# Kernel tuning notes

Measured on AMD Instinct MI355X. Metric: run time of the kernel, lower is better.

## Reference

```python
import jax, jax.numpy as jnp
import numpy as np


def setup_inputs() -> dict:
    key = jax.random.key(0)
    k1, k2 = jax.random.split(key)
    B, Lq, Ls, D = 16, 2048, 2048, 512
    query = jax.random.normal(k1, (B, Lq, D), dtype=jnp.float32)
    support = jax.random.normal(k2, (B, Ls, D), dtype=jnp.float32)
    return {"query": query, "support": support}


def reference(query, support):
    # attn: [B, Lq, Ls] = softmax(query @ support^T, axis=-1)
    logits = jnp.einsum("bqd,bsd->bqs", query, support)
    attn = jax.nn.softmax(logits, axis=-1)
    # attended support: [B, Lq, D]
    attended = jnp.einsum("bqs,bsd->bqd", attn, support)
    # score: [B, Lq] = sum over D of query * attended
    score = jnp.sum(query * attended, axis=-1)
    return score
```

## Files before the change

### kernel.cpp

```cpp
#include <hip/hip_runtime.h>
#include <hip/hip_bf16.h>

#define B_  16
#define LQ  2048
#define LS  2048
#define DD  512
#define BQ  128
#define BS  128
#define BK  64
#define NSB (LS / BS)
#define NKC (DD / BK)
#define NSPLIT 4

static_assert(NKC == 8, "stage>>3 math assumes NKC==8");

typedef short bf16x8 __attribute__((ext_vector_type(8)));
typedef float f32x4  __attribute__((ext_vector_type(4)));

__device__ __forceinline__ void load_lds16(const void* g, void* l) {
  __builtin_amdgcn_global_load_lds((const __attribute__((address_space(1))) void*)g,
                                   (__attribute__((address_space(3))) void*)l,
                                   16, 0, 0);
}

__device__ __forceinline__ unsigned short f2bf(float f) {
  union { float f; unsigned int u; } v; v.f = f;
  unsigned int r = v.u + 0x7fffu + ((v.u >> 16) & 1u);
  return (unsigned short)(r >> 16);
}

__global__ __launch_bounds__(256) void cvt_kernel(const float* __restrict__ Q,
                                                  const float* __restrict__ S,
                                                  unsigned short* __restrict__ Qw,
                                                  unsigned short* __restrict__ Sw,
                                                  int nblk) {
  int blk = blockIdx.x;
  const float* src; unsigned short* dst;
  if (blk < nblk) { src = Q; dst = Qw; } else { src = S; dst = Sw; blk -= nblk; }
  int i = blk * 256 + threadIdx.x;
  float4 f = ((const float4*)src)[i];
  ushort4 u;
  u.x = f2bf(f.x); u.y = f2bf(f.y); u.z = f2bf(f.z); u.w = f2bf(f.w);
  ((ushort4*)dst)[i] = u;
}

__global__ __launch_bounds__(512, 4) void attn_kernel(const unsigned short* __restrict__ Qw,
                                                      const unsigned short* __restrict__ Sw,
                                                      float* __restrict__ out,
                                                      float* __restrict__ pm,
                                                      float* __restrict__ pse,
                                                      float* __restrict__ psel,
                                                      int nsplit) {
  __shared__ __align__(16) unsigned short sQ[2][BQ * BK];
  __shared__ __align__(16) unsigned short sS[2][BS * BK];

  const int pid = blockIdx.x + (blockIdx.y << 4) + (blockIdx.z << 8);
  const int nch = (nsplit << 8) >> 3;
  const int lid = (pid & 7) * nch + (pid >> 3);
  const int qb  = lid & 15;
  const int b   = (lid >> 4) & 15;
  const int spl = lid >> 8;

  const int tid  = threadIdx.x;
  const int w    = tid >> 6;
  const int lane = tid & 63;
  const int h    = w & 1;
  const int g    = w >> 1;
  const int col  = lane & 15;
  const int quad = lane >> 4;
  const int c7   = col & 7;

  const int q0 = qb * BQ;
  const unsigned short* Qb = Qw + (size_t)b * LQ * DD;
  const unsigned short* Sb = Sw + (size_t)b * LS * DD;

  float mst[2] = { -INFINITY, -INFINITY };
  float se[2]  = { 0.f, 0.f };
  float sel[2] = { 0.f, 0.f };

  f32x4 acc[4][2];
#pragma unroll
  for (int st = 0; st < 4; ++st)
#pragma unroll
    for (int qt = 0; qt < 2; ++qt)
      acc[st][qt] = (f32x4){0.f, 0.f, 0.f, 0.f};

  const int rr    = lane >> 3;
  const int cc    = ((lane & 7) ^ rr) * 8;
  const int srow0 = (w & 3) * 32;

  const int sbs = spl * (NSB / nsplit);
  const int nst = (NSB / nsplit) * NKC;

  auto issue_stage = [&](int sb_i, int kc_i, int buf) {
    if (w < 4) {
#pragma unroll
      for (int i = 0; i < 4; ++i) {
        int r0 = srow0 + i * 8;
        load_lds16(Qb + (size_t)(q0 + r0 + rr) * DD + kc_i * BK + cc, &sQ[buf][r0 * BK]);
      }
    } else {
      const int s0i = sb_i * BS;
#pragma unroll
      for (int i = 0; i < 4; ++i) {
        int r0 = srow0 + i * 8;
        load_lds16(Sb + (size_t)(s0i + r0 + rr) * DD + kc_i * BK + cc, &sS[buf][r0 * BK]);
      }
    }
  };

  issue_stage(sbs, 0, 0);
  int cur = 0;

#pragma unroll 1
  for (int t = 0; t < nst; ++t) {
    asm volatile("s_waitcnt lgkmcnt(0)" ::: "memory");
    __builtin_amdgcn_s_barrier();

    const int tn = t + 1;
    if (tn < nst) {
      issue_stage(sbs + (tn >> 3), tn & 7, cur ^ 1);
      asm volatile("s_waitcnt vmcnt(4)" ::: "memory");
    } else {
      asm volatile("s_waitcnt vmcnt(0)" ::: "memory");
    }
    __builtin_amdgcn_s_barrier();
    __builtin_amdgcn_sched_barrier(0);

    const unsigned short* bq = &sQ[cur][0];
    const unsigned short* bs = &sS[cur][0];
    __builtin_amdgcn_s_setprio(1);
#pragma unroll
    for (int kk = 0; kk < 2; ++kk) {
      const int koff = ((kk * 4 + quad) ^ c7) * 8;
      bf16x8 aq[2], asv[4];
#pragma unroll
      for (int qt = 0; qt < 2; ++qt)
        aq[qt] = *(const bf16x8*)&bq[(g * 32 + qt * 16 + col) * BK + koff];
#pragma unroll
      for (int st = 0; st < 4; ++st)
        asv[st] = *(const bf16x8*)&bs[(h * 64 + st * 16 + col) * BK + koff];
#pragma unroll
      for (int st = 0; st < 4; ++st)
#pragma unroll
        for (int qt = 0; qt < 2; ++qt)
          acc[st][qt] = __builtin_amdgcn_mfma_f32_16x16x32_bf16(asv[st], aq[qt], acc[st][qt], 0, 0, 0);
    }
    __builtin_amdgcn_s_setprio(0);
    cur ^= 1;

    if ((t & (NKC - 1)) == NKC - 1) {
#pragma unroll
      for (int qt = 0; qt < 2; ++qt) {
        float lmax = mst[qt];
#pragma unroll
        for (int st = 0; st < 4; ++st)
#pragma unroll
          for (int r = 0; r < 4; ++r)
            lmax = fmaxf(lmax, acc[st][qt][r]);
        lmax = fmaxf(lmax, __shfl_xor(lmax, 16, 64));
        lmax = fmaxf(lmax, __shfl_xor(lmax, 32, 64));
        float alpha = __expf(mst[qt] - lmax);
        float pe = 0.f, pel = 0.f;
#pragma unroll
        for (int st = 0; st < 4; ++st)
#pragma unroll
          for (int r = 0; r < 4; ++r) {
            float l = acc[st][qt][r];
            float e = __expf(l - lmax);
            pe += e;
            pel = fmaf(e, l, pel);
          }
        pe  += __shfl_xor(pe, 16, 64);  pe  += __shfl_xor(pe, 32, 64);
        pel += __shfl_xor(pel, 16, 64); pel += __shfl_xor(pel, 32, 64);
        se[qt]  = fmaf(se[qt],  alpha, pe);
        sel[qt] = fmaf(sel[qt], alpha, pel);
        mst[qt] = lmax;
      }
#pragma unroll
      for (int st = 0; st < 4; ++st)
#pragma unroll
        for (int qt = 0; qt < 2; ++qt)
          acc[st][qt] = (f32x4){0.f, 0.f, 0.f, 0.f};
    }
  }

  __syncthreads();
  float* red = (float*)&sQ[0][0];
  if (quad == 0) {
#pragma unroll
    for (int qt = 0; qt < 2; ++qt) {
      int idx = ((g * 2 + h) * 2 + qt) * 16 + col;
      red[idx]       = mst[qt];
      red[256 + idx] = se[qt];
      red[512 + idx] = sel[qt];
    }
  }
  __syncthreads();
  if (h == 0 && quad == 0) {
#pragma unroll
    for (int qt = 0; qt < 2; ++qt) {
      int i0 = ((g * 2 + 0) * 2 + qt) * 16 + col;
      int i1 = ((g * 2 + 1) * 2 + qt) * 16 + col;
      float m0 = red[i0], m1 = red[i1];
      float M  = fmaxf(m0, m1);
      float a0 = __expf(m0 - M), a1 = __expf(m1 - M);
      float SE  = red[256 + i0] * a0 + red[256 + i1] * a1;
      float SEL = red[512 + i0] * a0 + red[512 + i1] * a1;
      size_t qi = (size_t)b * LQ + q0 + g * 32 + qt * 16 + col;
      if (nsplit == 1) {
        out[qi] = SEL / SE;
      } else {
        pm[qi * NSPLIT + spl]   = M;
        pse[qi * NSPLIT + spl]  = SE;
        psel[qi * NSPLIT + spl] = SEL;
      }
    }
  }
}

__global__ __launch_bounds__(256) void combine_kernel(const float* __restrict__ pm,
                                                      const float* __restrict__ pse,
                                                      const float* __restrict__ psel,
                                                      float* __restrict__ out) {
  int i = blockIdx.x * blockDim.x + threadIdx.x;
  if (i >= B_ * LQ) return;
  float M = -INFINITY;
#pragma unroll
  for (int s = 0; s < NSPLIT; ++s) M = fmaxf(M, pm[i * NSPLIT + s]);
  float SE = 0.f, SEL = 0.f;
#pragma unroll
  for (int s = 0; s < NSPLIT; ++s) {
    float a = __expf(pm[i * NSPLIT + s] - M);
    SE  = fmaf(pse[i * NSPLIT + s],  a, SE);
    SEL = fmaf(psel[i * NSPLIT + s], a, SEL);
  }
  out[i] = SEL / SE;
}

__global__ __launch_bounds__(256) void fallback_kernel(const float* __restrict__ Q,
                                                       const float* __restrict__ S,
                                                       float* __restrict__ out) {
  __shared__ float qv[DD];
  __shared__ float red[256];
  const int b = blockIdx.y, qi = blockIdx.x, tid = threadIdx.x;
  const float* qrow = Q + ((size_t)b * LQ + qi) * DD;
  for (int d = tid; d < DD; d += 256) qv[d] = qrow[d];
  __syncthreads();
  const float* Sb = S + (size_t)b * LS * DD;
  float m = -INFINITY, se = 0.f, sel = 0.f;
  for (int s = tid; s < LS; s += 256) {
    const float* srow = Sb + (size_t)s * DD;
    float dot = 0.f;
    for (int d = 0; d < DD; ++d) dot = fmaf(qv[d], srow[d], dot);
    float mn = fmaxf(m, dot);
    float a = __expf(m - mn);
    float e = __expf(dot - mn);
    se  = se * a + e;
    sel = sel * a + e * dot;
    m = mn;
  }
  red[tid] = m; __syncthreads();
  for (int o = 128; o > 0; o >>= 1) { if (tid < o) red[tid] = fmaxf(red[tid], red[tid + o]); __syncthreads(); }
  float M = red[0]; __syncthreads();
  float a = __expf(m - M); se *= a; sel *= a;
  red[tid] = se; __syncthreads();
  for (int o = 128; o > 0; o >>= 1) { if (tid < o) red[tid] += red[tid + o]; __syncthreads(); }
  float SE = red[0]; __syncthreads();
  red[tid] = sel; __syncthreads();
  for (int o = 128; o > 0; o >>= 1) { if (tid < o) red[tid] += red[tid + o]; __syncthreads(); }
  float SEL = red[0];
  if (tid == 0) out[(size_t)b * LQ + qi] = SEL / SE;
}

extern "C" void kernel_launch(void* const* d_in, const int* in_sizes, int n_in,
                              void* d_out, int out_size, void* d_ws, size_t ws_size,
                              hipStream_t stream) {
  const float* Q = (const float*)d_in[0];
  const float* S = (const float*)d_in[1];
  float* out = (float*)d_out;
  const size_t nelem = (size_t)B_ * LQ * DD;
  const size_t need_base  = 2 * nelem * sizeof(unsigned short);
  const size_t part_elems = (size_t)B_ * LQ * NSPLIT;
  const size_t need_split = need_base + 3 * part_elems * sizeof(float);

  if (ws_size >= need_base) {
    unsigned short* Qw = (unsigned short*)d_ws;
    unsigned short* Sw = Qw + nelem;
    int nblk = (int)(nelem / 4 / 256);
    cvt_kernel<<<2 * nblk, 256, 0, stream>>>(Q, S, Qw, Sw, nblk);
    if (ws_size >= need_split) {
      float* pm   = (float*)(Sw + nelem);
      float* pse  = pm + part_elems;
      float* psel = pse + part_elems;
      attn_kernel<<<dim3(LQ / BQ, B_, NSPLIT), 512, 0, stream>>>(Qw, Sw, out, pm, pse, psel, NSPLIT);
      combine_kernel<<<(B_ * LQ + 255) / 256, 256, 0, stream>>>(pm, pse, psel, out);
    } else {
      attn_kernel<<<dim3(LQ / BQ, B_, 1), 512, 0, stream>>>(Qw, Sw, out, nullptr, nullptr, nullptr, 1);
    }
  } else {
    fallback_kernel<<<dim3(LQ, B_), 256, 0, stream>>>(Q, S, out);
  }
}
```

Baseline: 234.8 us.

## Double the Q and S tile sizes to 256 with larger per-wave register tiles

Grows the block tile from 128x128 to 256x256, so each wave now holds an 8x4 grid of MFMA accumulators instead of 4x2. Each staged LDS chunk is reused for twice as many MFMAs, which cuts global and LDS traffic per FLOP. Launch bounds drop to 2 waves per SIMD, and the block-id decoding, load issue and reduction layout are reworked to match. In exchange, LDS use doubles to 128KB per block, so only one block fits per CU. Register pressure also rises sharply, which risks spills and less latency hiding.

```diff
diff --git a/kernel.cpp b/kernel.cpp
--- a/kernel.cpp
+++ b/kernel.cpp
@@ -5,8 +5,8 @@
 #define LQ  2048
 #define LS  2048
 #define DD  512
-#define BQ  128
-#define BS  128
+#define BQ  256
+#define BS  256
 #define BK  64
 #define NSB (LS / BS)
 #define NKC (DD / BK)
@@ -44,7 +44,7 @@
   ((ushort4*)dst)[i] = u;
 }
 
-__global__ __launch_bounds__(512, 4) void attn_kernel(const unsigned short* __restrict__ Qw,
+__global__ __launch_bounds__(512, 2) void attn_kernel(const unsigned short* __restrict__ Qw,
                                                       const unsigned short* __restrict__ Sw,
                                                       float* __restrict__ out,
                                                       float* __restrict__ pm,
@@ -54,12 +54,12 @@
   __shared__ __align__(16) unsigned short sQ[2][BQ * BK];
   __shared__ __align__(16) unsigned short sS[2][BS * BK];
 
-  const int pid = blockIdx.x + (blockIdx.y << 4) + (blockIdx.z << 8);
-  const int nch = (nsplit << 8) >> 3;
+  const int pid = blockIdx.x + (blockIdx.y << 3) + (blockIdx.z << 7);
+  const int nch = (nsplit << 7) >> 3;
   const int lid = (pid & 7) * nch + (pid >> 3);
-  const int qb  = lid & 15;
-  const int b   = (lid >> 4) & 15;
-  const int spl = lid >> 8;
+  const int qb  = lid & 7;
+  const int b   = (lid >> 3) & 15;
+  const int spl = lid >> 7;
 
   const int tid  = threadIdx.x;
   const int w    = tid >> 6;
@@ -74,42 +74,42 @@
   const unsigned short* Qb = Qw + (size_t)b * LQ * DD;
   const unsigned short* Sb = Sw + (size_t)b * LS * DD;
 
-  float mst[2] = { -INFINITY, -INFINITY };
-  float se[2]  = { 0.f, 0.f };
-  float sel[2] = { 0.f, 0.f };
-
-  f32x4 acc[4][2];
-#pragma unroll
-  for (int st = 0; st < 4; ++st)
-#pragma unroll
-    for (int qt = 0; qt < 2; ++qt)
+  float mst[4] = { -INFINITY, -INFINITY, -INFINITY, -INFINITY };
+  float se[4]  = { 0.f, 0.f, 0.f, 0.f };
+  float sel[4] = { 0.f, 0.f, 0.f, 0.f };
+
+  f32x4 acc[8][4];
+#pragma unroll
+  for (int st = 0; st < 8; ++st)
+#pragma unroll
+    for (int qt = 0; qt < 4; ++qt)
       acc[st][qt] = (f32x4){0.f, 0.f, 0.f, 0.f};
 
-  const int rr    = lane >> 3;
-  const int cc    = ((lane & 7) ^ rr) * 8;
-  const int srow0 = (w & 3) * 32;
+  const int rr = lane >> 3;
+  const int cc = ((lane & 7) ^ rr) * 8;
 
   const int sbs = spl * (NSB / nsplit);
   const int nst = (NSB / nsplit) * NKC;
 
-  auto issue_stage = [&](int sb_i, int kc_i, int buf) {
+  auto issue_stage = [&](int t_i, int buf) {
+    const int kc = t_i & 7;
     if (w < 4) {
-#pragma unroll
-      for (int i = 0; i < 4; ++i) {
-        int r0 = srow0 + i * 8;
-        load_lds16(Qb + (size_t)(q0 + r0 + rr) * DD + kc_i * BK + cc, &sQ[buf][r0 * BK]);
-      }
+      const unsigned short* gp = Qb + (size_t)(q0 + w * 64 + rr) * DD + kc * BK + cc;
+      unsigned short* lp = &sQ[buf][(w * 64) * BK];
+#pragma unroll
+      for (int i = 0; i < 8; ++i)
+        load_lds16(gp + (size_t)i * 8 * DD, lp + i * 8 * BK);
     } else {
-      const int s0i = sb_i * BS;
-#pragma unroll
-      for (int i = 0; i < 4; ++i) {
-        int r0 = srow0 + i * 8;
-        load_lds16(Sb + (size_t)(s0i + r0 + rr) * DD + kc_i * BK + cc, &sS[buf][r0 * BK]);
-      }
+      const int sb = sbs + (t_i >> 3);
+      const unsigned short* gp = Sb + (size_t)(sb * BS + (w - 4) * 64 + rr) * DD + kc * BK + cc;
+      unsigned short* lp = &sS[buf][((w - 4) * 64) * BK];
+#pragma unroll
+      for (int i = 0; i < 8; ++i)
+        load_lds16(gp + (size_t)i * 8 * DD, lp + i * 8 * BK);
     }
   };
 
-  issue_stage(sbs, 0, 0);
+  issue_stage(0, 0);
   int cur = 0;
 
 #pragma unroll 1
@@ -119,8 +119,8 @@
 
     const int tn = t + 1;
     if (tn < nst) {
-      issue_stage(sbs + (tn >> 3), tn & 7, cur ^ 1);
-      asm volatile("s_waitcnt vmcnt(4)" ::: "memory");
+      issue_stage(tn, cur ^ 1);
+      asm volatile("s_waitcnt vmcnt(8)" ::: "memory");
     } else {
       asm volatile("s_waitcnt vmcnt(0)" ::: "memory");
     }
@@ -133,28 +133,27 @@
 #pragma unroll
     for (int kk = 0; kk < 2; ++kk) {
       const int koff = ((kk * 4 + quad) ^ c7) * 8;
-      bf16x8 aq[2], asv[4];
-#pragma unroll
-      for (int qt = 0; qt < 2; ++qt)
-        aq[qt] = *(const bf16x8*)&bq[(g * 32 + qt * 16 + col) * BK + koff];
-#pragma unroll
-      for (int st = 0; st < 4; ++st)
-        asv[st] = *(const bf16x8*)&bs[(h * 64 + st * 16 + col) * BK + koff];
-#pragma unroll
-      for (int st = 0; st < 4; ++st)
-#pragma unroll
-        for (int qt = 0; qt < 2; ++qt)
-          acc[st][qt] = __builtin_amdgcn_mfma_f32_16x16x32_bf16(asv[st], aq[qt], acc[st][qt], 0, 0, 0);
+      bf16x8 asv[8];
+#pragma unroll
+      for (int st = 0; st < 8; ++st)
+        asv[st] = *(const bf16x8*)&bs[(h * 128 + st * 16 + col) * BK + koff];
+#pragma unroll
+      for (int qt = 0; qt < 4; ++qt) {
+        bf16x8 aq = *(const bf16x8*)&bq[(g * 64 + qt * 16 + col) * BK + koff];
+#pragma unroll
+        for (int st = 0; st < 8; ++st)
+          acc[st][qt] = __builtin_amdgcn_mfma_f32_16x16x32_bf16(asv[st], aq, acc[st][qt], 0, 0, 0);
+      }
     }
     __builtin_amdgcn_s_setprio(0);
     cur ^= 1;
 
     if ((t & (NKC - 1)) == NKC - 1) {
 #pragma unroll
-      for (int qt = 0; qt < 2; ++qt) {
+      for (int qt = 0; qt < 4; ++qt) {
         float lmax = mst[qt];
 #pragma unroll
-        for (int st = 0; st < 4; ++st)
+        for (int st = 0; st < 8; ++st)
 #pragma unroll
           for (int r = 0; r < 4; ++r)
             lmax = fmaxf(lmax, acc[st][qt][r]);
@@ -163,7 +162,7 @@
         float alpha = __expf(mst[qt] - lmax);
         float pe = 0.f, pel = 0.f;
 #pragma unroll
-        for (int st = 0; st < 4; ++st)
+        for (int st = 0; st < 8; ++st)
 #pragma unroll
           for (int r = 0; r < 4; ++r) {
             float l = acc[st][qt][r];
@@ -176,12 +175,10 @@
         se[qt]  = fmaf(se[qt],  alpha, pe);
         sel[qt] = fmaf(sel[qt], alpha, pel);
         mst[qt] = lmax;
+#pragma unroll
+        for (int st = 0; st < 8; ++st)
+          acc[st][qt] = (f32x4){0.f, 0.f, 0.f, 0.f};
       }
-#pragma unroll
-      for (int st = 0; st < 4; ++st)
-#pragma unroll
-        for (int qt = 0; qt < 2; ++qt)
-          acc[st][qt] = (f32x4){0.f, 0.f, 0.f, 0.f};
     }
   }
 
@@ -189,25 +186,24 @@
   float* red = (float*)&sQ[0][0];
   if (quad == 0) {
 #pragma unroll
-    for (int qt = 0; qt < 2; ++qt) {
-      int idx = ((g * 2 + h) * 2 + qt) * 16 + col;
-      red[idx]       = mst[qt];
-      red[256 + idx] = se[qt];
-      red[512 + idx] = sel[qt];
+    for (int qt = 0; qt < 4; ++qt) {
+      int qq = g * 64 + qt * 16 + col;
+      red[h * 256 + qq]        = mst[qt];
+      red[512 + h * 256 + qq]  = se[qt];
+      red[1024 + h * 256 + qq] = sel[qt];
     }
   }
   __syncthreads();
   if (h == 0 && quad == 0) {
 #pragma unroll
-    for (int qt = 0; qt < 2; ++qt) {
-      int i0 = ((g * 2 + 0) * 2 + qt) * 16 + col;
-      int i1 = ((g * 2 + 1) * 2 + qt) * 16 + col;
-      float m0 = red[i0], m1 = red[i1];
+    for (int qt = 0; qt < 4; ++qt) {
+      int qq = g * 64 + qt * 16 + col;
+      float m0 = red[qq],       m1 = red[256 + qq];
       float M  = fmaxf(m0, m1);
       float a0 = __expf(m0 - M), a1 = __expf(m1 - M);
-      float SE  = red[256 + i0] * a0 + red[256 + i1] * a1;
-      float SEL = red[512 + i0] * a0 + red[512 + i1] * a1;
-      size_t qi = (size_t)b * LQ + q0 + g * 32 + qt * 16 + col;
+      float SE  = red[512 + qq]  * a0 + red[512 + 256 + qq]  * a1;
+      float SEL = red[1024 + qq] * a0 + red[1024 + 256 + qq] * a1;
+      size_t qi = (size_t)b * LQ + q0 + qq;
       if (nsplit == 1) {
         out[qi] = SEL / SE;
       } else {
```

Result: faster. 221.3 us (-5.7%).
